# Kernel optimization log

Measured on AMD Instinct MI355X. Metric: run time of the kernel, lower is better.

## Reference

```python
import jax, jax.numpy as jnp
import numpy as np

N_USERS = 60000
N_ITEMS = 40000
N_NORM = 60000          # n_norm_users == n_users
D = 64                  # embedding_size
L = 3                   # n_layers
N_INTER = 1000000       # training interactions
B = 4096                # bpr batch
N_NODES = N_USERS + N_ITEMS          # 100000
FEAT_DIM = N_NORM + N_ITEMS + 2      # 100002


def setup_inputs() -> dict:
    rng = np.random.default_rng(0)
    u = rng.integers(0, N_USERS, N_INTER)
    it = rng.integers(0, N_ITEMS, N_INTER)
    # feat_mat edges (generate_feat): (user, N_NORM+item), (N_USERS+item, user),
    # plus per-user bias col N_NORM+N_ITEMS and per-item bias col N_NORM+N_ITEMS+1
    feat_row = np.concatenate([u, N_USERS + it, np.arange(N_USERS), N_USERS + np.arange(N_ITEMS)])
    feat_col = np.concatenate([N_NORM + it, u,
                               np.full(N_USERS, N_NORM + N_ITEMS),
                               np.full(N_ITEMS, N_NORM + N_ITEMS + 1)])
    # symmetric bipartite adjacency (generate_daj_mat)
    adj_row = np.concatenate([u, N_USERS + it])
    adj_col = np.concatenate([N_USERS + it, u])
    key = jax.random.key(0)
    k1, k2, k3, k4 = jax.random.split(key, 4)
    emb = jax.random.normal(k1, (FEAT_DIM, D), dtype=jnp.float32) * 0.1  # normal_(std=0.1)
    users = jax.random.randint(k2, (B,), 0, N_USERS)
    pos_items = jax.random.randint(k3, (B,), 0, N_ITEMS)
    neg_items = jax.random.randint(k4, (B,), 0, N_ITEMS)
    return {"emb": emb,
            "feat_row": jnp.asarray(feat_row, dtype=jnp.int64),
            "feat_col": jnp.asarray(feat_col, dtype=jnp.int64),
            "adj_row": jnp.asarray(adj_row, dtype=jnp.int64),
            "adj_col": jnp.asarray(adj_col, dtype=jnp.int64),
            "users": users, "pos_items": pos_items, "neg_items": neg_items}


def _spmm(vals, row, col, x, num_segments):
    # out[row] += vals * x[col]  (gspmm 'mul','sum' on graph (col->row))
    return jax.ops.segment_sum(x[col] * vals[:, None], row, num_segments=num_segments)


def reference(emb, feat_row, feat_col, adj_row, adj_col, users, pos_items, neg_items):
    ones_f = jnp.ones(feat_row.shape, dtype=jnp.float32)
    feat_deg = jax.ops.segment_sum(ones_f, feat_row, num_segments=N_NODES)  # row sums of feat_mat
    feat_vals = 1.0 / feat_deg[feat_row]
    # inductive_rep_layer: x = D_row^{-1} feat_mat @ emb  (padding rows never indexed)
    x = _spmm(feat_vals, feat_row, feat_col, emb, N_NODES)

    ones_a = jnp.ones(adj_row.shape, dtype=jnp.float32)
    adj_deg = jax.ops.segment_sum(ones_a, adj_row, num_segments=N_NODES)
    v = adj_deg[adj_row] ** -0.5 * adj_deg[adj_col] ** -0.5
    v = jnp.where(jnp.isinf(v), 1.0, v)

    rep = x
    acc = x
    for _ in range(L):  # fixed small layer count
        rep = _spmm(v, adj_row, adj_col, rep, N_NODES)
        acc = acc + rep
    final_rep = acc / jnp.float32(L + 1)  # mean over stacked layers

    users_r = final_rep[users]
    pos_r = final_rep[N_USERS + pos_items]
    neg_r = final_rep[N_USERS + neg_items]
    l2 = (users_r ** 2).sum(-1) + (pos_r ** 2).sum(-1) + (neg_r ** 2).sum(-1)
    return users_r, pos_r, neg_r, l2
```

## Files before the change

kernel.cpp:

```cpp
#include <hip/hip_runtime.h>
#include <hip/hip_fp16.h>


constexpr int kNU = 60000;
constexpr int kNI = 40000;
constexpr int kN  = 100000;
constexpr int kB  = 4096;
constexpr int NR  = 8,  RSZ = 12500;
constexpr int NC  = 64;

struct alignas(16) H8 { __half2 h[4]; };
struct alignas(8)  H4 { __half2 lo, hi; };

__global__ void hist_k(const int4* __restrict__ u4, const int4* __restrict__ i4,
                       int nV, int* __restrict__ hist) {
  int r = blockIdx.x & (NR - 1), c = blockIdx.x >> 3;
  int lo = r * RSZ;
  __shared__ int h[RSZ];
  for (int i = threadIdx.x; i < RSZ; i += 256) h[i] = 0;
  __syncthreads();
  int cl = (nV + NC - 1) / NC;
  int p0 = c * cl, p1 = min(nV, p0 + cl);
  for (int p = p0 + (int)threadIdx.x; p < p1; p += 256) {
    int4 uu = u4[p], ii = i4[p];
    int a;
    a = uu.x - lo; if ((unsigned)a < (unsigned)RSZ) atomicAdd(&h[a], 1);
    a = ii.x - lo; if ((unsigned)a < (unsigned)RSZ) atomicAdd(&h[a], 1);
    a = uu.y - lo; if ((unsigned)a < (unsigned)RSZ) atomicAdd(&h[a], 1);
    a = ii.y - lo; if ((unsigned)a < (unsigned)RSZ) atomicAdd(&h[a], 1);
    a = uu.z - lo; if ((unsigned)a < (unsigned)RSZ) atomicAdd(&h[a], 1);
    a = ii.z - lo; if ((unsigned)a < (unsigned)RSZ) atomicAdd(&h[a], 1);
    a = uu.w - lo; if ((unsigned)a < (unsigned)RSZ) atomicAdd(&h[a], 1);
    a = ii.w - lo; if ((unsigned)a < (unsigned)RSZ) atomicAdd(&h[a], 1);
  }
  __syncthreads();
  int* dst = hist + (long)(r * NC + c) * RSZ;
  for (int i = threadIdx.x; i < RSZ; i += 256) dst[i] = h[i];
}

__global__ void degsum_k(const int* __restrict__ hist, int* __restrict__ deg,
                         float* __restrict__ rsDg) {
  int row = blockIdx.x * 256 + threadIdx.x;
  if (row >= kN) return;
  int r = row / RSZ, local = row - r * RSZ;
  const int* base = hist + (long)r * NC * RSZ + local;
  int s = 0;
  for (int c = 0; c < NC; ++c) s += base[(long)c * RSZ];
  deg[row] = s;
  rsDg[row] = s > 0 ? rsqrtf((float)s) : 1.f;
}

constexpr int SCAN_T = 256, SCAN_E = 8, SCAN_CH = SCAN_T * SCAN_E;

__global__ void scan_p1(const int* __restrict__ in, int n, int* __restrict__ bsum) {
  __shared__ int lds[SCAN_T];
  int t = threadIdx.x;
  int base = blockIdx.x * SCAN_CH + t * SCAN_E;
  int s = 0;
  #pragma unroll
  for (int k = 0; k < SCAN_E; ++k) { int i = base + k; if (i < n) s += in[i]; }
  lds[t] = s; __syncthreads();
  for (int off = SCAN_T / 2; off; off >>= 1) {
    if (t < off) lds[t] += lds[t + off];
    __syncthreads();
  }
  if (t == 0) bsum[blockIdx.x] = lds[0];
}

__global__ void scan_p2(int* bsum, int nb) {
  if (threadIdx.x == 0 && blockIdx.x == 0) {
    int run = 0;
    for (int i = 0; i < nb; ++i) { int v = bsum[i]; bsum[i] = run; run += v; }
  }
}

__global__ void scan_p3(const int* __restrict__ in, int n, int ntot,
                        const int* __restrict__ bsum, int* __restrict__ out) {
  __shared__ int lds[SCAN_T];
  int t = threadIdx.x;
  int base = blockIdx.x * SCAN_CH + t * SCAN_E;
  int v[SCAN_E]; int s = 0;
  #pragma unroll
  for (int k = 0; k < SCAN_E; ++k) { int i = base + k; v[k] = (i < n) ? in[i] : 0; s += v[k]; }
  lds[t] = s; __syncthreads();
  for (int off = 1; off < SCAN_T; off <<= 1) {
    int x = (t >= off) ? lds[t - off] : 0;
    __syncthreads();
    lds[t] += x;
    __syncthreads();
  }
  int pre = lds[t] - s + bsum[blockIdx.x];
  #pragma unroll
  for (int k = 0; k < SCAN_E; ++k) {
    int i = base + k;
    if (i < n) { out[i] = pre; pre += v[k]; }
  }
  if (blockIdx.x == 0 && t == 0) out[n] = ntot;
}

__global__ void expand_k(int* __restrict__ hist, const int* __restrict__ rowStart) {
  int row = blockIdx.x * 256 + threadIdx.x;
  if (row >= kN) return;
  int r = row / RSZ, local = row - r * RSZ;
  int* base = hist + (long)r * NC * RSZ + local;
  int run = rowStart[row];
  for (int c = 0; c < NC; ++c) {
    long idx = (long)c * RSZ;
    int v = base[idx];
    base[idx] = run;
    run += v;
  }
}

__global__ void scatter_h(const int4* __restrict__ u4, const int4* __restrict__ i4,
                          int nV, const int* __restrict__ hist,
                          unsigned short* __restrict__ cols) {
  int r = blockIdx.x & (NR - 1), c = blockIdx.x >> 3;
  int lo = r * RSZ;
  __shared__ int pf[RSZ];
  const int* src = hist + (long)(r * NC + c) * RSZ;
  for (int i = threadIdx.x; i < RSZ; i += 256) pf[i] = src[i];
  __syncthreads();
  int cl = (nV + NC - 1) / NC;
  int p0 = c * cl, p1 = min(nV, p0 + cl);
  for (int p = p0 + (int)threadIdx.x; p < p1; p += 256) {
    int4 uu = u4[p], ii = i4[p];
    int a, pos;
    a = uu.x - lo; if ((unsigned)a < (unsigned)RSZ) { pos = atomicAdd(&pf[a], 1); cols[pos] = (unsigned short)(ii.x - kNU); }
    a = ii.x - lo; if ((unsigned)a < (unsigned)RSZ) { pos = atomicAdd(&pf[a], 1); cols[pos] = (unsigned short)uu.x; }
    a = uu.y - lo; if ((unsigned)a < (unsigned)RSZ) { pos = atomicAdd(&pf[a], 1); cols[pos] = (unsigned short)(ii.y - kNU); }
    a = ii.y - lo; if ((unsigned)a < (unsigned)RSZ) { pos = atomicAdd(&pf[a], 1); cols[pos] = (unsigned short)uu.y; }
    a = uu.z - lo; if ((unsigned)a < (unsigned)RSZ) { pos = atomicAdd(&pf[a], 1); cols[pos] = (unsigned short)(ii.z - kNU); }
    a = ii.z - lo; if ((unsigned)a < (unsigned)RSZ) { pos = atomicAdd(&pf[a], 1); cols[pos] = (unsigned short)uu.z; }
    a = uu.w - lo; if ((unsigned)a < (unsigned)RSZ) { pos = atomicAdd(&pf[a], 1); cols[pos] = (unsigned short)(ii.w - kNU); }
    a = ii.w - lo; if ((unsigned)a < (unsigned)RSZ) { pos = atomicAdd(&pf[a], 1); cols[pos] = (unsigned short)uu.w; }
  }
}

__global__ void emb_to_h(const float4* __restrict__ in, H4* __restrict__ outp, int n) {
  int i = blockIdx.x * 256 + threadIdx.x;
  if (i < n) {
    float4 v = in[i];
    float2 lo = {v.x, v.y}, hi = {v.z, v.w};
    H4 o; o.lo = __float22half2_rn(lo); o.hi = __float22half2_rn(hi);
    outp[i] = o;
  }
}

__global__ void spmm_feat_all(const int* __restrict__ rs, const unsigned short* __restrict__ cols,
                              const H8* __restrict__ emb16, const float* __restrict__ rsDg,
                              H8* __restrict__ hU, H8* __restrict__ hI) {
  int row = blockIdx.x * 4 + (threadIdx.x >> 6);
  if (row >= kN) return;
  int lane = threadIdx.x & 63, g = lane >> 3, q = lane & 7;
  int s = rs[row], e = rs[row + 1];
  int base = (row < kNU) ? kNU : 0;
  __half2 z = __float2half2_rn(0.f);
  __half2 hacc[4] = {z, z, z, z};
  int j = s + g;
  for (; j + 8 < e; j += 16) {
    int c0 = cols[j], c1 = cols[j + 8];
    H8 v0 = emb16[(long)(base + c0) * 8 + q];
    H8 v1 = emb16[(long)(base + c1) * 8 + q];
    #pragma unroll
    for (int k = 0; k < 4; ++k)
      hacc[k] = __hadd2(hacc[k], __hadd2(v0.h[k], v1.h[k]));
  }
  if (j < e) {
    int c = cols[j];
    H8 v = emb16[(long)(base + c) * 8 + q];
    #pragma unroll
    for (int k = 0; k < 4; ++k) hacc[k] = __hadd2(hacc[k], v.h[k]);
  }
  float a[8];
  #pragma unroll
  for (int k = 0; k < 4; ++k) {
    float2 f = __half22float2(hacc[k]);
    a[2 * k] = f.x; a[2 * k + 1] = f.y;
  }
  #pragma unroll
  for (int m = 8; m <= 32; m <<= 1) {
    #pragma unroll
    for (int k = 0; k < 8; ++k) a[k] += __shfl_xor(a[k], m, 64);
  }
  if (g == 0) {
    H8 bv = emb16[(long)((row < kNU) ? 100000 : 100001) * 8 + q];
    float sc = rsDg[row] / (float)(e - s + 1);
    H8 o;
    #pragma unroll
    for (int k = 0; k < 4; ++k) {
      float2 bf = __half22float2(bv.h[k]);
      float2 f = {(a[2 * k] + bf.x) * sc, (a[2 * k + 1] + bf.y) * sc};
      o.h[k] = __float22half2_rn(f);
    }
    H8* dst = (row < kNU) ? (hU + (long)row * 8) : (hI + (long)(row - kNU) * 8);
    dst[q] = o;
  }
}

__global__ void spmm_adj_all(const int* __restrict__ rs, const unsigned short* __restrict__ cols,
                             const float* __restrict__ rsDg,
                             const H8* __restrict__ inU, const H8* __restrict__ inI,
                             H8* __restrict__ outU, H8* __restrict__ outI) {
  int row = blockIdx.x * 4 + (threadIdx.x >> 6);
  if (row >= kN) return;
  int lane = threadIdx.x & 63, g = lane >> 3, q = lane & 7;
  const H8* src = (row < kNU) ? inI : inU;
  int s = rs[row], e = rs[row + 1];
  __half2 z = __float2half2_rn(0.f);
  __half2 hacc[4] = {z, z, z, z};
  int j = s + g;
  for (; j + 8 < e; j += 16) {
    int c0 = cols[j], c1 = cols[j + 8];
    H8 v0 = src[(long)c0 * 8 + q];
    H8 v1 = src[(long)c1 * 8 + q];
    #pragma unroll
    for (int k = 0; k < 4; ++k)
      hacc[k] = __hadd2(hacc[k], __hadd2(v0.h[k], v1.h[k]));
  }
  if (j < e) {
    int c = cols[j];
    H8 v = src[(long)c * 8 + q];
    #pragma unroll
    for (int k = 0; k < 4; ++k) hacc[k] = __hadd2(hacc[k], v.h[k]);
  }
  float a[8];
  #pragma unroll
  for (int k = 0; k < 4; ++k) {
    float2 f = __half22float2(hacc[k]);
    a[2 * k] = f.x; a[2 * k + 1] = f.y;
  }
  #pragma unroll
  for (int m = 8; m <= 32; m <<= 1) {
    #pragma unroll
    for (int k = 0; k < 8; ++k) a[k] += __shfl_xor(a[k], m, 64);
  }
  if (g == 0) {
    float w = rsDg[row]; w = w * w;
    H8 o;
    #pragma unroll
    for (int k = 0; k < 4; ++k) {
      float2 f = {a[2 * k] * w, a[2 * k + 1] * w};
      o.h[k] = __float22half2_rn(f);
    }
    H8* dst = (row < kNU) ? (outU + (long)row * 8) : (outI + (long)(row - kNU) * 8);
    dst[q] = o;
  }
}

__global__ void acc_gather_h(const H8* __restrict__ hU, const H8* __restrict__ hI,
                             const int* __restrict__ deg,
                             const int* __restrict__ users, const int* __restrict__ pos,
                             const int* __restrict__ neg, float4* __restrict__ out, int add) {
  int gI = blockIdx.x * blockDim.x + threadIdx.x;
  if (gI >= 3 * kB * 8) return;
  int slot = gI >> 3, q = gI & 7;
  int which = slot >> 12, b = slot & (kB - 1);
  int node = which == 0 ? users[b] : (which == 1 ? pos[b] + kNU : neg[b] + kNU);
  H8 v = (node < kNU) ? hU[(long)node * 8 + q] : hI[(long)(node - kNU) * 8 + q];
  float sq = sqrtf((float)max(deg[node], 1));
  float2 f0 = __half22float2(v.h[0]), f1 = __half22float2(v.h[1]);
  float2 f2 = __half22float2(v.h[2]), f3 = __half22float2(v.h[3]);
  float4 r0 = {f0.x * sq, f0.y * sq, f1.x * sq, f1.y * sq};
  float4 r1 = {f2.x * sq, f2.y * sq, f3.x * sq, f3.y * sq};
  long o0 = (long)slot * 16 + q * 2;
  if (add) {
    float4 a0 = out[o0], a1 = out[o0 + 1];
    r0.x += a0.x; r0.y += a0.y; r0.z += a0.z; r0.w += a0.w;
    r1.x += a1.x; r1.y += a1.y; r1.z += a1.z; r1.w += a1.w;
  }
  out[o0] = r0; out[o0 + 1] = r1;
}

__global__ void layer3_fin(const int* __restrict__ rs, const unsigned short* __restrict__ cols,
                           const float* __restrict__ rsDg,
                           const H8* __restrict__ hU, const H8* __restrict__ hI,
                           const int* __restrict__ users, const int* __restrict__ pos,
                           const int* __restrict__ neg,
                           float4* __restrict__ out, float* __restrict__ l2part) {
  int slot = blockIdx.x * 4 + (threadIdx.x >> 6);
  if (slot >= 3 * kB) return;
  int lane = threadIdx.x & 63, g = lane >> 3, q = lane & 7;
  int which = slot >> 12, b = slot & (kB - 1);
  int node = which == 0 ? users[b] : (which == 1 ? pos[b] + kNU : neg[b] + kNU);
  const H8* src = (node < kNU) ? hI : hU;
  int s = rs[node], e = rs[node + 1];
  __half2 z = __float2half2_rn(0.f);
  __half2 hacc[4] = {z, z, z, z};
  int j = s + g;
  for (; j + 8 < e; j += 16) {
    int c0 = cols[j], c1 = cols[j + 8];
    H8 v0 = src[(long)c0 * 8 + q];
    H8 v1 = src[(long)c1 * 8 + q];
    #pragma unroll
    for (int k = 0; k < 4; ++k)
      hacc[k] = __hadd2(hacc[k], __hadd2(v0.h[k], v1.h[k]));
  }
  if (j < e) {
    int c = cols[j];
    H8 v = src[(long)c * 8 + q];
    #pragma unroll
    for (int k = 0; k < 4; ++k) hacc[k] = __hadd2(hacc[k], v.h[k]);
  }
  float a[8];
  #pragma unroll
  for (int k = 0; k < 4; ++k) {
    float2 f = __half22float2(hacc[k]);
    a[2 * k] = f.x; a[2 * k + 1] = f.y;
  }
  #pragma unroll
  for (int m = 8; m <= 32; m <<= 1) {
    #pragma unroll
    for (int k = 0; k < 8; ++k) a[k] += __shfl_xor(a[k], m, 64);
  }
  float t = 0.f;
  if (g == 0) {
    float sr = rsDg[node];
    long o0 = (long)slot * 16 + q * 2;
    float4 a0 = out[o0], a1 = out[o0 + 1];
    float4 r0 = {(a0.x + a[0] * sr) * 0.25f, (a0.y + a[1] * sr) * 0.25f,
                 (a0.z + a[2] * sr) * 0.25f, (a0.w + a[3] * sr) * 0.25f};
    float4 r1 = {(a1.x + a[4] * sr) * 0.25f, (a1.y + a[5] * sr) * 0.25f,
                 (a1.z + a[6] * sr) * 0.25f, (a1.w + a[7] * sr) * 0.25f};
    out[o0] = r0; out[o0 + 1] = r1;
    t = r0.x * r0.x + r0.y * r0.y + r0.z * r0.z + r0.w * r0.w
      + r1.x * r1.x + r1.y * r1.y + r1.z * r1.z + r1.w * r1.w;
  }
  #pragma unroll
  for (int m = 1; m <= 4; m <<= 1) t += __shfl_xor(t, m, 64);
  if (lane == 0) l2part[slot] = t;
}

__global__ void l2_final(const float* __restrict__ l2part, float* __restrict__ outl2) {
  int b = blockIdx.x * blockDim.x + threadIdx.x;
  if (b < kB) outl2[b] = l2part[b] + l2part[kB + b] + l2part[2 * kB + b];
}

extern "C" void kernel_launch(void* const* d_in, const int* in_sizes, int n_in,
                              void* d_out, int out_size, void* d_ws, size_t ws_size,
                              hipStream_t stream) {
  const float* emb  = (const float*)d_in[0];
  const int*   arow = (const int*)d_in[3];
  const int*   users= (const int*)d_in[5];
  const int*   pos  = (const int*)d_in[6];
  const int*   neg  = (const int*)d_in[7];
  const int neA = in_sizes[3];
  const int nP  = neA / 2;
  const int nV  = nP / 4;
  const int4* u4 = (const int4*)arow;
  const int4* i4 = (const int4*)(arow + nP);

  char* ws = (char*)d_ws;
  int*            degA     = (int*)(ws + 0);
  int*            rowStart = (int*)(ws + 400000);
  float*          rsDg     = (float*)(ws + 800128);
  float*          l2part   = (float*)(ws + 1200128);
  int*            bsum     = (int*)(ws + 1249280);
  unsigned short* colA     = (unsigned short*)(ws + 1250304);
  __half*         emb16    = (__half*)(ws + 5250304);
  int*            hist     = (int*)(ws + 18050560);
  __half*         hU0      = (__half*)(ws + 18050560);
  __half*         hU1      = (__half*)(ws + 25730560);
  __half*         hI0      = (__half*)(ws + 33410560);
  __half*         hI1      = (__half*)(ws + 38530560);

  float* out = (float*)d_out;
  const int NB = (kN + SCAN_CH - 1) / SCAN_CH;
  const int RG = (kN + 255) / 256;

  hist_k<<<NR * NC, 256, 0, stream>>>(u4, i4, nV, hist);
  degsum_k<<<RG, 256, 0, stream>>>(hist, degA, rsDg);
  scan_p1<<<NB, SCAN_T, 0, stream>>>(degA, kN, bsum);
  scan_p2<<<1, 64, 0, stream>>>(bsum, NB);
  scan_p3<<<NB, SCAN_T, 0, stream>>>(degA, kN, neA, bsum, rowStart);
  const int nE16 = 100002 * 16;
  emb_to_h<<<(nE16 + 255) / 256, 256, 0, stream>>>((const float4*)emb, (H4*)emb16, nE16);
  expand_k<<<RG, 256, 0, stream>>>(hist, rowStart);
  scatter_h<<<NR * NC, 256, 0, stream>>>(u4, i4, nV, hist, colA);

  const int GN = (kN + 3) / 4;

  spmm_feat_all<<<GN, 256, 0, stream>>>(rowStart, colA, (const H8*)emb16, rsDg,
                                        (H8*)hU0, (H8*)hI0);
  acc_gather_h<<<(3 * kB * 8 + 255) / 256, 256, 0, stream>>>((const H8*)hU0, (const H8*)hI0,
      degA, users, pos, neg, (float4*)out, 0);

  spmm_adj_all<<<GN, 256, 0, stream>>>(rowStart, colA, rsDg, (const H8*)hU0, (const H8*)hI0,
                                       (H8*)hU1, (H8*)hI1);
  acc_gather_h<<<(3 * kB * 8 + 255) / 256, 256, 0, stream>>>((const H8*)hU1, (const H8*)hI1,
      degA, users, pos, neg, (float4*)out, 1);

  spmm_adj_all<<<GN, 256, 0, stream>>>(rowStart, colA, rsDg, (const H8*)hU1, (const H8*)hI1,
                                       (H8*)hU0, (H8*)hI0);
  acc_gather_h<<<(3 * kB * 8 + 255) / 256, 256, 0, stream>>>((const H8*)hU0, (const H8*)hI0,
      degA, users, pos, neg, (float4*)out, 1);

  layer3_fin<<<(3 * kB + 3) / 4, 256, 0, stream>>>(rowStart, colA, rsDg, (const H8*)hU0,
                                                   (const H8*)hI0, users, pos, neg,
                                                   (float4*)out, l2part);
  l2_final<<<(kB + 255) / 256, 256, 0, stream>>>(l2part, out + 3 * kB * 64);
}
```

Baseline: 223.8 us.

## Map one row per 8-lane group in SpMM kernels, removing cross-lane reductions

Both SpMM kernels now assign each row to an 8-lane subgroup (8 rows per wavefront, 32 per block) instead of a full 64-lane wavefront with 8 edge groups. Each subgroup walks its row's edges serially, two at a time, which removes the shuffle-xor reduction and the idle lanes during writeback. The catch is load imbalance inside a wavefront when row degrees differ. Also, each lane now issues more dependent gathers per row, so latency hiding depends on occupancy.

```diff
diff --git a/kernel.cpp b/kernel.cpp
--- a/kernel.cpp
+++ b/kernel.cpp
@@ -150,16 +150,17 @@
 __global__ void spmm_feat_all(const int* __restrict__ rs, const unsigned short* __restrict__ cols,
                               const H8* __restrict__ emb16, const float* __restrict__ rsDg,
                               H8* __restrict__ hU, H8* __restrict__ hI) {
-  int row = blockIdx.x * 4 + (threadIdx.x >> 6);
+  int lane = threadIdx.x & 63, wid = threadIdx.x >> 6;
+  int rg = lane >> 3, q = lane & 7;
+  int row = blockIdx.x * 32 + wid * 8 + rg;
   if (row >= kN) return;
-  int lane = threadIdx.x & 63, g = lane >> 3, q = lane & 7;
   int s = rs[row], e = rs[row + 1];
   int base = (row < kNU) ? kNU : 0;
   __half2 z = __float2half2_rn(0.f);
   __half2 hacc[4] = {z, z, z, z};
-  int j = s + g;
-  for (; j + 8 < e; j += 16) {
-    int c0 = cols[j], c1 = cols[j + 8];
+  int j = s;
+  for (; j + 1 < e; j += 2) {
+    int c0 = cols[j], c1 = cols[j + 1];
     H8 v0 = emb16[(long)(base + c0) * 8 + q];
     H8 v1 = emb16[(long)(base + c1) * 8 + q];
     #pragma unroll
@@ -172,46 +173,35 @@
     #pragma unroll
     for (int k = 0; k < 4; ++k) hacc[k] = __hadd2(hacc[k], v.h[k]);
   }
-  float a[8];
+  H8 bv = emb16[(long)((row < kNU) ? 100000 : 100001) * 8 + q];
+  float sc = rsDg[row] / (float)(e - s + 1);
+  H8 o;
   #pragma unroll
   for (int k = 0; k < 4; ++k) {
     float2 f = __half22float2(hacc[k]);
-    a[2 * k] = f.x; a[2 * k + 1] = f.y;
-  }
-  #pragma unroll
-  for (int m = 8; m <= 32; m <<= 1) {
-    #pragma unroll
-    for (int k = 0; k < 8; ++k) a[k] += __shfl_xor(a[k], m, 64);
-  }
-  if (g == 0) {
-    H8 bv = emb16[(long)((row < kNU) ? 100000 : 100001) * 8 + q];
-    float sc = rsDg[row] / (float)(e - s + 1);
-    H8 o;
-    #pragma unroll
-    for (int k = 0; k < 4; ++k) {
-      float2 bf = __half22float2(bv.h[k]);
-      float2 f = {(a[2 * k] + bf.x) * sc, (a[2 * k + 1] + bf.y) * sc};
-      o.h[k] = __float22half2_rn(f);
-    }
-    H8* dst = (row < kNU) ? (hU + (long)row * 8) : (hI + (long)(row - kNU) * 8);
-    dst[q] = o;
-  }
+    float2 bf = __half22float2(bv.h[k]);
+    float2 r = {(f.x + bf.x) * sc, (f.y + bf.y) * sc};
+    o.h[k] = __float22half2_rn(r);
+  }
+  if (row < kNU) hU[(long)row * 8 + q] = o;
+  else           hI[(long)(row - kNU) * 8 + q] = o;
 }
 
 __global__ void spmm_adj_all(const int* __restrict__ rs, const unsigned short* __restrict__ cols,
                              const float* __restrict__ rsDg,
                              const H8* __restrict__ inU, const H8* __restrict__ inI,
                              H8* __restrict__ outU, H8* __restrict__ outI) {
-  int row = blockIdx.x * 4 + (threadIdx.x >> 6);
+  int lane = threadIdx.x & 63, wid = threadIdx.x >> 6;
+  int rg = lane >> 3, q = lane & 7;
+  int row = blockIdx.x * 32 + wid * 8 + rg;
   if (row >= kN) return;
-  int lane = threadIdx.x & 63, g = lane >> 3, q = lane & 7;
   const H8* src = (row < kNU) ? inI : inU;
   int s = rs[row], e = rs[row + 1];
   __half2 z = __float2half2_rn(0.f);
   __half2 hacc[4] = {z, z, z, z};
-  int j = s + g;
-  for (; j + 8 < e; j += 16) {
-    int c0 = cols[j], c1 = cols[j + 8];
+  int j = s;
+  for (; j + 1 < e; j += 2) {
+    int c0 = cols[j], c1 = cols[j + 1];
     H8 v0 = src[(long)c0 * 8 + q];
     H8 v1 = src[(long)c1 * 8 + q];
     #pragma unroll
@@ -224,28 +214,16 @@
     #pragma unroll
     for (int k = 0; k < 4; ++k) hacc[k] = __hadd2(hacc[k], v.h[k]);
   }
-  float a[8];
+  float w = rsDg[row]; w = w * w;
+  H8 o;
   #pragma unroll
   for (int k = 0; k < 4; ++k) {
     float2 f = __half22float2(hacc[k]);
-    a[2 * k] = f.x; a[2 * k + 1] = f.y;
-  }
-  #pragma unroll
-  for (int m = 8; m <= 32; m <<= 1) {
-    #pragma unroll
-    for (int k = 0; k < 8; ++k) a[k] += __shfl_xor(a[k], m, 64);
-  }
-  if (g == 0) {
-    float w = rsDg[row]; w = w * w;
-    H8 o;
-    #pragma unroll
-    for (int k = 0; k < 4; ++k) {
-      float2 f = {a[2 * k] * w, a[2 * k + 1] * w};
-      o.h[k] = __float22half2_rn(f);
-    }
-    H8* dst = (row < kNU) ? (outU + (long)row * 8) : (outI + (long)(row - kNU) * 8);
-    dst[q] = o;
-  }
+    float2 r = {f.x * w, f.y * w};
+    o.h[k] = __float22half2_rn(r);
+  }
+  if (row < kNU) outU[(long)row * 8 + q] = o;
+  else           outI[(long)(row - kNU) * 8 + q] = o;
 }
 
 __global__ void acc_gather_h(const H8* __restrict__ hU, const H8* __restrict__ hI,
@@ -378,7 +356,7 @@
   expand_k<<<RG, 256, 0, stream>>>(hist, rowStart);
   scatter_h<<<NR * NC, 256, 0, stream>>>(u4, i4, nV, hist, colA);
 
-  const int GN = (kN + 3) / 4;
+  const int GN = (kN + 31) / 32;
 
   spmm_feat_all<<<GN, 256, 0, stream>>>(rowStart, colA, (const H8*)emb16, rsDg,
                                         (H8*)hU0, (H8*)hI0);
```

Result: faster. 193.8 us (median of 2 runs) (-13.4%).
